# Performance work log

Measured on AMD Instinct MI355X. Metric: run time of the kernel, lower is better.

## Reference

```python
import jax, jax.numpy as jnp
import numpy as np

HIDDEN = 2048
N_HEADS = 32
N_KV_HEADS = 8
N_GROUPS = N_HEADS // N_KV_HEADS  # 4
HEAD_DIM = HIDDEN // N_HEADS      # 64
BATCH, SEQ = 2, 2048


def setup_inputs() -> dict:
    key = jax.random.key(0)
    ks = jax.random.split(key, 5)
    s = 0.02
    return {
        "x": jax.random.normal(ks[0], (BATCH, SEQ, HIDDEN), dtype=jnp.float32),
        "Wq": jax.random.normal(ks[1], (HIDDEN, HIDDEN), dtype=jnp.float32) * s,
        "Wk": jax.random.normal(ks[2], (N_KV_HEADS * HEAD_DIM, HIDDEN), dtype=jnp.float32) * s,
        "Wv": jax.random.normal(ks[3], (N_KV_HEADS * HEAD_DIM, HIDDEN), dtype=jnp.float32) * s,
        "Wo": jax.random.normal(ks[4], (HIDDEN, HIDDEN), dtype=jnp.float32) * s,
    }


def reference(x, Wq, Wk, Wv, Wo):
    b, s, _ = x.shape
    # Projections (nn.Linear: y = x @ W.T)
    q = (x @ Wq.T).reshape(b, s, N_KV_HEADS, N_GROUPS, HEAD_DIM)  # group heads by kv head
    k = (x @ Wk.T).reshape(b, s, N_KV_HEADS, HEAD_DIM)
    v = (x @ Wv.T).reshape(b, s, N_KV_HEADS, HEAD_DIM)
    scale = 1.0 / jnp.sqrt(jnp.asarray(HEAD_DIM, dtype=x.dtype))
    # Grouped scores: equivalent to repeat_interleave of K over groups
    scores = jnp.einsum('bqhgd,bkhd->bhgqk', q, k) * scale  # [b, kvh, g, s, s]
    causal_mask = jnp.triu(jnp.ones((s, s), dtype=bool), k=1)
    scores = jnp.where(causal_mask, -jnp.inf, scores)
    attn = jax.nn.softmax(scores, axis=-1)
    out = jnp.einsum('bhgqk,bkhd->bqhgd', attn, v)  # [b, s, kvh, g, hd]
    out = out.reshape(b, s, HIDDEN)
    return out @ Wo.T
```

## Files before the change

kernel.cpp:

```cpp
#include <hip/hip_runtime.h>

#define HIDDEN 2048
#define NHEADS 32
#define NKV 8
#define HD 64
#define BATCH 2
#define SEQ 2048
#define MROWS (BATCH*SEQ)
#define KVDIM (NKV*HD)
#define QKVN (HIDDEN + 2*KVDIM)

typedef __bf16 bf16x8 __attribute__((ext_vector_type(8)));
typedef float f32x4 __attribute__((ext_vector_type(4)));

__device__ inline void gld16(const __bf16* g, __bf16* l) {
    __builtin_amdgcn_global_load_lds((const __attribute__((address_space(1))) void*)g,
                                     (__attribute__((address_space(3))) void*)l, 16, 0, 0);
}

__global__ __launch_bounds__(256) void cast_all(const float* __restrict__ x,
                                                const float* __restrict__ wq,
                                                const float* __restrict__ wk,
                                                const float* __restrict__ wv,
                                                const float* __restrict__ wo,
                                                __bf16* __restrict__ xb,
                                                __bf16* __restrict__ wqkv,
                                                __bf16* __restrict__ wob,
                                                float qscale) {
    int blk = blockIdx.x;
    const float* src; __bf16* dst; float sc = 1.0f; size_t off;
    if (blk < 8192)        { src = x;  dst = xb;   off = (size_t)blk * 1024; }
    else if (blk < 12288)  { src = wq; dst = wqkv; off = (size_t)(blk - 8192) * 1024; sc = qscale; }
    else if (blk < 13312)  { src = wk; dst = wqkv + (size_t)HIDDEN * HIDDEN; off = (size_t)(blk - 12288) * 1024; }
    else if (blk < 14336)  { src = wv; dst = wqkv + (size_t)(HIDDEN + KVDIM) * HIDDEN; off = (size_t)(blk - 13312) * 1024; }
    else                   { src = wo; dst = wob;  off = (size_t)(blk - 14336) * 1024; }
    size_t i4 = off + (size_t)threadIdx.x * 4;
    float4 f = *(const float4*)(src + i4);
    dst[i4 + 0] = (__bf16)(f.x * sc);
    dst[i4 + 1] = (__bf16)(f.y * sc);
    dst[i4 + 2] = (__bf16)(f.z * sc);
    dst[i4 + 3] = (__bf16)(f.w * sc);
}

__device__ inline void store_val(__bf16* C, size_t idx, float v) { C[idx] = (__bf16)v; }
__device__ inline void store_val(float* C, size_t idx, float v) { C[idx] = v; }

template <typename OutT>
__global__ __launch_bounds__(256) void gemm128(const __bf16* __restrict__ A,
                                               const __bf16* __restrict__ B,
                                               OutT* __restrict__ C,
                                               int M, int N, int K) {
    __shared__ __bf16 As[2][128][32];
    __shared__ __bf16 Bs[2][128][32];
    const int tid  = threadIdx.x;
    const int lane = tid & 63;
    const int w    = tid >> 6;
    const int col  = lane & 15;
    const int quad = lane >> 4;
    const int m0 = blockIdx.y * 128;
    const int n0 = blockIdx.x * 128;
    const int wm = (w >> 1) * 64;
    const int wn = (w & 1) * 64;

    f32x4 acc[4][4];
    #pragma unroll
    for (int i = 0; i < 4; i++)
        #pragma unroll
        for (int j = 0; j < 4; j++) acc[i][j] = (f32x4){0.f,0.f,0.f,0.f};

    const int lrow = lane >> 2;
    const int lcol = (lane & 3) * 8;

    auto stage = [&](int k0, int buf) {
        #pragma unroll
        for (int c = 0; c < 4; c++) {
            int chunk = w * 4 + c;
            if (chunk < 8) {
                const __bf16* g = A + (size_t)(m0 + chunk*16 + lrow) * K + k0 + lcol;
                gld16(g, &As[buf][chunk*16][0]);
            } else {
                int bc = chunk - 8;
                const __bf16* g = B + (size_t)(n0 + bc*16 + lrow) * K + k0 + lcol;
                gld16(g, &Bs[buf][bc*16][0]);
            }
        }
    };

    const int nk = K / 32;
    stage(0, 0);
    for (int ki = 0; ki < nk; ki++) {
        const int buf = ki & 1;
        __syncthreads();
        if (ki + 1 < nk) stage((ki + 1) * 32, buf ^ 1);

        bf16x8 af[4], bfr[4];
        #pragma unroll
        for (int i = 0; i < 4; i++) af[i]  = *(const bf16x8*)&As[buf][wm + i*16 + col][quad*8];
        #pragma unroll
        for (int j = 0; j < 4; j++) bfr[j] = *(const bf16x8*)&Bs[buf][wn + j*16 + col][quad*8];
        #pragma unroll
        for (int i = 0; i < 4; i++)
            #pragma unroll
            for (int j = 0; j < 4; j++)
                acc[i][j] = __builtin_amdgcn_mfma_f32_16x16x32_bf16(af[i], bfr[j], acc[i][j], 0, 0, 0);
    }

    #pragma unroll
    for (int i = 0; i < 4; i++) {
        #pragma unroll
        for (int r = 0; r < 4; r++) {
            int mrow = m0 + wm + i*16 + quad*4 + r;
            size_t base = (size_t)mrow * N + n0 + wn;
            #pragma unroll
            for (int j = 0; j < 4; j++)
                store_val(C, base + j*16 + col, acc[i][j][r]);
        }
    }
}

__global__ __launch_bounds__(256) void transpose_v(const __bf16* __restrict__ QKV,
                                                   __bf16* __restrict__ VT) {
    __shared__ __bf16 tile[64][72];
    const int r0 = blockIdx.x * 64;
    const int s0 = blockIdx.y * 64;
    const int t  = threadIdx.x;
    #pragma unroll
    for (int cc = 0; cc < 2; cc++) {
        int c = t + cc * 256;
        int i = c >> 3;
        int j8 = (c & 7) * 8;
        bf16x8 v = *(const bf16x8*)(QKV + (size_t)(s0 + i) * QKVN + (HIDDEN + KVDIM) + r0 + j8);
        *(bf16x8*)&tile[i][j8] = v;
    }
    __syncthreads();
    #pragma unroll
    for (int cc = 0; cc < 2; cc++) {
        int c = t + cc * 256;
        int d = c >> 3;
        int sc = (c & 7) * 8;
        bf16x8 vv;
        #pragma unroll
        for (int j = 0; j < 8; j++) vv[j] = tile[sc + j][d];
        *(bf16x8*)(VT + (size_t)(r0 + d) * MROWS + s0 + sc) = vv;
    }
}

__global__ __launch_bounds__(256) void flash_attn(const __bf16* __restrict__ QKV,
                                                  const __bf16* __restrict__ VT,
                                                  __bf16* __restrict__ O) {
    const int p    = blockIdx.x & 15;
    const int head = (blockIdx.x >> 4) & 31;
    const int b    = blockIdx.x >> 9;
    const int kvh  = head >> 2;
    const int tid  = threadIdx.x;
    const int lane = tid & 63;
    const int w    = tid >> 6;
    const int col  = lane & 15;
    const int quad = lane >> 4;

    const int qbL = p * 64 + w * 16;
    const int qbH = (31 - p) * 64 + w * 16;
    const int np  = p + 1;
    const int nh  = 32 - p;

    __shared__ __bf16 Ks[2][64][32];
    __shared__ __bf16 Vs[2][64][32];
    __shared__ __bf16 Pt[4][32][72];

    const size_t qL = (size_t)(b * SEQ + qbL + col) * QKVN + head * HD;
    const size_t qH = (size_t)(b * SEQ + qbH + col) * QKVN + head * HD;
    bf16x8 aqL0 = *(const bf16x8*)(QKV + qL + quad * 8);
    bf16x8 aqL1 = *(const bf16x8*)(QKV + qL + 32 + quad * 8);
    bf16x8 aqH0 = *(const bf16x8*)(QKV + qH + quad * 8);
    bf16x8 aqH1 = *(const bf16x8*)(QKV + qH + 32 + quad * 8);

    bf16x8 ones;
    #pragma unroll
    for (int j = 0; j < 8; j++) ones[j] = (__bf16)1.0f;

    f32x4 oL[4], oH[4];
    #pragma unroll
    for (int dn = 0; dn < 4; dn++) { oL[dn] = (f32x4){0.f,0.f,0.f,0.f}; oH[dn] = (f32x4){0.f,0.f,0.f,0.f}; }
    f32x4 lsumL = (f32x4){0.f,0.f,0.f,0.f};
    f32x4 lsumH = (f32x4){0.f,0.f,0.f,0.f};

    const int lrow = lane >> 2;
    const int lcol = (lane & 3) * 8;

    for (int kt = 0; kt < nh; kt++) {
        const int kbase = kt * 64;
        const bool dual = (kt < np);
        __syncthreads();
        #pragma unroll
        for (int c = 0; c < 4; c++) {
            int chunk = w * 4 + c;
            if (chunk < 8) {
                int h = chunk >> 2, rb = chunk & 3;
                const __bf16* g = QKV + (size_t)(b * SEQ + kbase + rb*16 + lrow) * QKVN
                                      + HIDDEN + kvh * HD + h * 32 + lcol;
                gld16(g, &Ks[h][rb*16][0]);
            } else {
                int vc = chunk - 8; int h = vc >> 2, db = vc & 3;
                const __bf16* g = VT + (size_t)(kvh * HD + db*16 + lrow) * MROWS
                                     + b * SEQ + kbase + h * 32 + lcol;
                gld16(g, &Vs[h][db*16][0]);
            }
        }
        __syncthreads();

        f32x4 sH[4], sL[4];
        #pragma unroll
        for (int j = 0; j < 4; j++) { sH[j] = (f32x4){0.f,0.f,0.f,0.f}; sL[j] = (f32x4){0.f,0.f,0.f,0.f}; }
        #pragma unroll
        for (int j = 0; j < 4; j++) {
            bf16x8 bk0 = *(const bf16x8*)&Ks[0][j*16 + col][quad*8];
            bf16x8 bk1 = *(const bf16x8*)&Ks[1][j*16 + col][quad*8];
            sH[j] = __builtin_amdgcn_mfma_f32_16x16x32_bf16(aqH0, bk0, sH[j], 0, 0, 0);
            sH[j] = __builtin_amdgcn_mfma_f32_16x16x32_bf16(aqH1, bk1, sH[j], 0, 0, 0);
            if (dual) {
                sL[j] = __builtin_amdgcn_mfma_f32_16x16x32_bf16(aqL0, bk0, sL[j], 0, 0, 0);
                sL[j] = __builtin_amdgcn_mfma_f32_16x16x32_bf16(aqL1, bk1, sL[j], 0, 0, 0);
            }
        }

        if (kt == nh - 1) {
            #pragma unroll
            for (int r = 0; r < 4; r++) {
                int qrow = qbH + quad*4 + r;
                #pragma unroll
                for (int j = 0; j < 4; j++)
                    if (kbase + j*16 + col > qrow) sH[j][r] = -1e30f;
            }
        }
        if (dual && kt == np - 1) {
            #pragma unroll
            for (int r = 0; r < 4; r++) {
                int qrow = qbL + quad*4 + r;
                #pragma unroll
                for (int j = 0; j < 4; j++)
                    if (kbase + j*16 + col > qrow) sL[j][r] = -1e30f;
            }
        }

        #pragma unroll
        for (int r = 0; r < 4; r++) {
            int pr = quad*4 + r;
            #pragma unroll
            for (int j = 0; j < 4; j++)
                Pt[w][pr][j*16 + col] = (__bf16)__builtin_amdgcn_exp2f(sH[j][r]);
        }
        if (dual) {
            #pragma unroll
            for (int r = 0; r < 4; r++) {
                int pr = quad*4 + r;
                #pragma unroll
                for (int j = 0; j < 4; j++)
                    Pt[w][16 + pr][j*16 + col] = (__bf16)__builtin_amdgcn_exp2f(sL[j][r]);
            }
        }

        __asm__ volatile("s_waitcnt lgkmcnt(0)" ::: "memory");
        bf16x8 apH0 = *(const bf16x8*)&Pt[w][col][quad*8];
        bf16x8 apH1 = *(const bf16x8*)&Pt[w][col][32 + quad*8];
        lsumH = __builtin_amdgcn_mfma_f32_16x16x32_bf16(apH0, ones, lsumH, 0, 0, 0);
        lsumH = __builtin_amdgcn_mfma_f32_16x16x32_bf16(apH1, ones, lsumH, 0, 0, 0);
        bf16x8 apL0, apL1;
        if (dual) {
            apL0 = *(const bf16x8*)&Pt[w][16 + col][quad*8];
            apL1 = *(const bf16x8*)&Pt[w][16 + col][32 + quad*8];
            lsumL = __builtin_amdgcn_mfma_f32_16x16x32_bf16(apL0, ones, lsumL, 0, 0, 0);
            lsumL = __builtin_amdgcn_mfma_f32_16x16x32_bf16(apL1, ones, lsumL, 0, 0, 0);
        }

        #pragma unroll
        for (int dn = 0; dn < 4; dn++) {
            bf16x8 bv0 = *(const bf16x8*)&Vs[0][dn*16 + col][quad*8];
            bf16x8 bv1 = *(const bf16x8*)&Vs[1][dn*16 + col][quad*8];
            oH[dn] = __builtin_amdgcn_mfma_f32_16x16x32_bf16(apH0, bv0, oH[dn], 0, 0, 0);
            oH[dn] = __builtin_amdgcn_mfma_f32_16x16x32_bf16(apH1, bv1, oH[dn], 0, 0, 0);
            if (dual) {
                oL[dn] = __builtin_amdgcn_mfma_f32_16x16x32_bf16(apL0, bv0, oL[dn], 0, 0, 0);
                oL[dn] = __builtin_amdgcn_mfma_f32_16x16x32_bf16(apL1, bv1, oL[dn], 0, 0, 0);
            }
        }
    }

    #pragma unroll
    for (int r = 0; r < 4; r++) {
        float invL = 1.0f / lsumL[r];
        float invH = 1.0f / lsumH[r];
        __bf16* opL = O + (size_t)(b * SEQ + qbL + quad*4 + r) * HIDDEN + head * HD;
        __bf16* opH = O + (size_t)(b * SEQ + qbH + quad*4 + r) * HIDDEN + head * HD;
        #pragma unroll
        for (int dn = 0; dn < 4; dn++) {
            opL[dn*16 + col] = (__bf16)(oL[dn][r] * invL);
            opH[dn*16 + col] = (__bf16)(oH[dn][r] * invH);
        }
    }
}

extern "C" void kernel_launch(void* const* d_in, const int* in_sizes, int n_in,
                              void* d_out, int out_size, void* d_ws, size_t ws_size,
                              hipStream_t stream) {
    const float* x  = (const float*)d_in[0];
    const float* Wq = (const float*)d_in[1];
    const float* Wk = (const float*)d_in[2];
    const float* Wv = (const float*)d_in[3];
    const float* Wo = (const float*)d_in[4];
    float* out = (float*)d_out;

    __bf16* p    = (__bf16*)d_ws;
    __bf16* xb   = p; p += (size_t)MROWS * HIDDEN;
    __bf16* wqkv = p; p += (size_t)QKVN * HIDDEN;
    __bf16* wob  = p; p += (size_t)HIDDEN * HIDDEN;
    __bf16* qkv  = p; p += (size_t)MROWS * QKVN;
    __bf16* vt   = p; p += (size_t)KVDIM * MROWS;
    __bf16* aob  = xb;

    const float qscale = 0.125f * 1.4426950408889634f;
    cast_all<<<18432, 256, 0, stream>>>(x, Wq, Wk, Wv, Wo, xb, wqkv, wob, qscale);

    dim3 blk(256);
    gemm128<__bf16><<<dim3(QKVN/128, MROWS/128), blk, 0, stream>>>(xb, wqkv, qkv, MROWS, QKVN, HIDDEN);
    transpose_v<<<dim3(KVDIM/64, MROWS/64), blk, 0, stream>>>(qkv, vt);
    flash_attn<<<BATCH * NHEADS * (SEQ/128), blk, 0, stream>>>(qkv, vt, aob);
    gemm128<float><<<dim3(HIDDEN/128, MROWS/128), blk, 0, stream>>>(aob, wob, out, MROWS, HIDDEN, HIDDEN);
}
```

Before: 324.9 us.

## Split attention KV loop across two blocks and merge partials in a combine kernel

Each query block's KV tiles are now split between two blocks (even and odd tiles), which doubles the grid for more parallelism and shortens each block's serial loop. Each block writes unnormalized bf16 partial outputs and row sums, and a new combine kernel adds the two partials and normalizes. The score computation is also restructured into a per-phase lambda with a smaller P tile in LDS and an occupancy hint in the launch bounds. The cost is an extra kernel launch, extra global traffic for the partial outputs, and bf16 rounding of the unnormalized partials.

```diff
diff --git a/kernel.cpp b/kernel.cpp
--- a/kernel.cpp
+++ b/kernel.cpp
@@ -145,12 +145,14 @@
     }
 }
 
-__global__ __launch_bounds__(256) void flash_attn(const __bf16* __restrict__ QKV,
-                                                  const __bf16* __restrict__ VT,
-                                                  __bf16* __restrict__ O) {
-    const int p    = blockIdx.x & 15;
-    const int head = (blockIdx.x >> 4) & 31;
-    const int b    = blockIdx.x >> 9;
+__global__ __launch_bounds__(256, 6) void flash_attn(const __bf16* __restrict__ QKV,
+                                                     const __bf16* __restrict__ VT,
+                                                     __bf16* __restrict__ OP,
+                                                     float* __restrict__ LP) {
+    const int e    = blockIdx.x & 1;
+    const int p    = (blockIdx.x >> 1) & 15;
+    const int head = (blockIdx.x >> 5) & 31;
+    const int b    = blockIdx.x >> 10;
     const int kvh  = head >> 2;
     const int tid  = threadIdx.x;
     const int lane = tid & 63;
@@ -165,14 +167,15 @@
 
     __shared__ __bf16 Ks[2][64][32];
     __shared__ __bf16 Vs[2][64][32];
-    __shared__ __bf16 Pt[4][32][72];
-
-    const size_t qL = (size_t)(b * SEQ + qbL + col) * QKVN + head * HD;
-    const size_t qH = (size_t)(b * SEQ + qbH + col) * QKVN + head * HD;
-    bf16x8 aqL0 = *(const bf16x8*)(QKV + qL + quad * 8);
-    bf16x8 aqL1 = *(const bf16x8*)(QKV + qL + 32 + quad * 8);
-    bf16x8 aqH0 = *(const bf16x8*)(QKV + qH + quad * 8);
-    bf16x8 aqH1 = *(const bf16x8*)(QKV + qH + 32 + quad * 8);
+    __shared__ __bf16 Pt[4][16][72];
+
+    const size_t bS = (size_t)b * SEQ;
+    const size_t qLg = (bS + qbL + col) * QKVN + head * HD;
+    const size_t qHg = (bS + qbH + col) * QKVN + head * HD;
+    bf16x8 aqL0 = *(const bf16x8*)(QKV + qLg + quad * 8);
+    bf16x8 aqL1 = *(const bf16x8*)(QKV + qLg + 32 + quad * 8);
+    bf16x8 aqH0 = *(const bf16x8*)(QKV + qHg + quad * 8);
+    bf16x8 aqH1 = *(const bf16x8*)(QKV + qHg + 32 + quad * 8);
 
     bf16x8 ones;
     #pragma unroll
@@ -187,116 +190,116 @@
     const int lrow = lane >> 2;
     const int lcol = (lane & 3) * 8;
 
-    for (int kt = 0; kt < nh; kt++) {
-        const int kbase = kt * 64;
-        const bool dual = (kt < np);
-        __syncthreads();
+    auto stage = [&](int kbase) {
         #pragma unroll
         for (int c = 0; c < 4; c++) {
             int chunk = w * 4 + c;
             if (chunk < 8) {
                 int h = chunk >> 2, rb = chunk & 3;
-                const __bf16* g = QKV + (size_t)(b * SEQ + kbase + rb*16 + lrow) * QKVN
+                const __bf16* g = QKV + (bS + kbase + rb*16 + lrow) * QKVN
                                       + HIDDEN + kvh * HD + h * 32 + lcol;
                 gld16(g, &Ks[h][rb*16][0]);
             } else {
                 int vc = chunk - 8; int h = vc >> 2, db = vc & 3;
                 const __bf16* g = VT + (size_t)(kvh * HD + db*16 + lrow) * MROWS
-                                     + b * SEQ + kbase + h * 32 + lcol;
+                                     + bS + kbase + h * 32 + lcol;
                 gld16(g, &Vs[h][db*16][0]);
             }
         }
-        __syncthreads();
-
-        f32x4 sH[4], sL[4];
-        #pragma unroll
-        for (int j = 0; j < 4; j++) { sH[j] = (f32x4){0.f,0.f,0.f,0.f}; sL[j] = (f32x4){0.f,0.f,0.f,0.f}; }
-        #pragma unroll
-        for (int j = 0; j < 4; j++) {
-            bf16x8 bk0 = *(const bf16x8*)&Ks[0][j*16 + col][quad*8];
-            bf16x8 bk1 = *(const bf16x8*)&Ks[1][j*16 + col][quad*8];
-            sH[j] = __builtin_amdgcn_mfma_f32_16x16x32_bf16(aqH0, bk0, sH[j], 0, 0, 0);
-            sH[j] = __builtin_amdgcn_mfma_f32_16x16x32_bf16(aqH1, bk1, sH[j], 0, 0, 0);
-            if (dual) {
-                sL[j] = __builtin_amdgcn_mfma_f32_16x16x32_bf16(aqL0, bk0, sL[j], 0, 0, 0);
-                sL[j] = __builtin_amdgcn_mfma_f32_16x16x32_bf16(aqL1, bk1, sL[j], 0, 0, 0);
-            }
-        }
-
-        if (kt == nh - 1) {
+    };
+
+    auto phase = [&](bf16x8 aq0, bf16x8 aq1, int qb, bool do_mask, int kbase,
+                     f32x4* o, f32x4& lsum) {
+        #pragma unroll
+        for (int jj = 0; jj < 2; jj++) {
+            f32x4 s[2];
+            s[0] = (f32x4){0.f,0.f,0.f,0.f};
+            s[1] = (f32x4){0.f,0.f,0.f,0.f};
             #pragma unroll
-            for (int r = 0; r < 4; r++) {
-                int qrow = qbH + quad*4 + r;
+            for (int jz = 0; jz < 2; jz++) {
+                int j = jj*2 + jz;
+                bf16x8 bk0 = *(const bf16x8*)&Ks[0][j*16 + col][quad*8];
+                bf16x8 bk1 = *(const bf16x8*)&Ks[1][j*16 + col][quad*8];
+                s[jz] = __builtin_amdgcn_mfma_f32_16x16x32_bf16(aq0, bk0, s[jz], 0, 0, 0);
+                s[jz] = __builtin_amdgcn_mfma_f32_16x16x32_bf16(aq1, bk1, s[jz], 0, 0, 0);
+            }
+            if (do_mask) {
                 #pragma unroll
-                for (int j = 0; j < 4; j++)
-                    if (kbase + j*16 + col > qrow) sH[j][r] = -1e30f;
-            }
-        }
-        if (dual && kt == np - 1) {
-            #pragma unroll
-            for (int r = 0; r < 4; r++) {
-                int qrow = qbL + quad*4 + r;
-                #pragma unroll
-                for (int j = 0; j < 4; j++)
-                    if (kbase + j*16 + col > qrow) sL[j][r] = -1e30f;
-            }
-        }
-
-        #pragma unroll
-        for (int r = 0; r < 4; r++) {
-            int pr = quad*4 + r;
-            #pragma unroll
-            for (int j = 0; j < 4; j++)
-                Pt[w][pr][j*16 + col] = (__bf16)__builtin_amdgcn_exp2f(sH[j][r]);
-        }
-        if (dual) {
+                for (int r = 0; r < 4; r++) {
+                    int qrow = qb + quad*4 + r;
+                    #pragma unroll
+                    for (int jz = 0; jz < 2; jz++)
+                        if (kbase + (jj*2+jz)*16 + col > qrow) s[jz][r] = -1e30f;
+                }
+            }
             #pragma unroll
             for (int r = 0; r < 4; r++) {
                 int pr = quad*4 + r;
-                #pragma unroll
-                for (int j = 0; j < 4; j++)
-                    Pt[w][16 + pr][j*16 + col] = (__bf16)__builtin_amdgcn_exp2f(sL[j][r]);
-            }
-        }
-
+                Pt[w][pr][(jj*2)*16 + col]   = (__bf16)__builtin_amdgcn_exp2f(s[0][r]);
+                Pt[w][pr][(jj*2+1)*16 + col] = (__bf16)__builtin_amdgcn_exp2f(s[1][r]);
+            }
+        }
         __asm__ volatile("s_waitcnt lgkmcnt(0)" ::: "memory");
-        bf16x8 apH0 = *(const bf16x8*)&Pt[w][col][quad*8];
-        bf16x8 apH1 = *(const bf16x8*)&Pt[w][col][32 + quad*8];
-        lsumH = __builtin_amdgcn_mfma_f32_16x16x32_bf16(apH0, ones, lsumH, 0, 0, 0);
-        lsumH = __builtin_amdgcn_mfma_f32_16x16x32_bf16(apH1, ones, lsumH, 0, 0, 0);
-        bf16x8 apL0, apL1;
-        if (dual) {
-            apL0 = *(const bf16x8*)&Pt[w][16 + col][quad*8];
-            apL1 = *(const bf16x8*)&Pt[w][16 + col][32 + quad*8];
-            lsumL = __builtin_amdgcn_mfma_f32_16x16x32_bf16(apL0, ones, lsumL, 0, 0, 0);
-            lsumL = __builtin_amdgcn_mfma_f32_16x16x32_bf16(apL1, ones, lsumL, 0, 0, 0);
-        }
-
+        bf16x8 ap0 = *(const bf16x8*)&Pt[w][col][quad*8];
+        bf16x8 ap1 = *(const bf16x8*)&Pt[w][col][32 + quad*8];
+        lsum = __builtin_amdgcn_mfma_f32_16x16x32_bf16(ap0, ones, lsum, 0, 0, 0);
+        lsum = __builtin_amdgcn_mfma_f32_16x16x32_bf16(ap1, ones, lsum, 0, 0, 0);
         #pragma unroll
         for (int dn = 0; dn < 4; dn++) {
             bf16x8 bv0 = *(const bf16x8*)&Vs[0][dn*16 + col][quad*8];
             bf16x8 bv1 = *(const bf16x8*)&Vs[1][dn*16 + col][quad*8];
-            oH[dn] = __builtin_amdgcn_mfma_f32_16x16x32_bf16(apH0, bv0, oH[dn], 0, 0, 0);
-            oH[dn] = __builtin_amdgcn_mfma_f32_16x16x32_bf16(apH1, bv1, oH[dn], 0, 0, 0);
-            if (dual) {
-                oL[dn] = __builtin_amdgcn_mfma_f32_16x16x32_bf16(apL0, bv0, oL[dn], 0, 0, 0);
-                oL[dn] = __builtin_amdgcn_mfma_f32_16x16x32_bf16(apL1, bv1, oL[dn], 0, 0, 0);
-            }
-        }
-    }
-
+            o[dn] = __builtin_amdgcn_mfma_f32_16x16x32_bf16(ap0, bv0, o[dn], 0, 0, 0);
+            o[dn] = __builtin_amdgcn_mfma_f32_16x16x32_bf16(ap1, bv1, o[dn], 0, 0, 0);
+        }
+    };
+
+    for (int kt = e; kt < nh; kt += 2) {
+        const int kbase = kt * 64;
+        __syncthreads();
+        stage(kbase);
+        __syncthreads();
+        phase(aqH0, aqH1, qbH, kt == nh - 1, kbase, oH, lsumH);
+        if (kt < np)
+            phase(aqL0, aqL1, qbL, kt == np - 1, kbase, oL, lsumL);
+    }
+
+    const size_t eoff = (size_t)e * MROWS * HIDDEN;
     #pragma unroll
     for (int r = 0; r < 4; r++) {
-        float invL = 1.0f / lsumL[r];
-        float invH = 1.0f / lsumH[r];
-        __bf16* opL = O + (size_t)(b * SEQ + qbL + quad*4 + r) * HIDDEN + head * HD;
-        __bf16* opH = O + (size_t)(b * SEQ + qbH + quad*4 + r) * HIDDEN + head * HD;
+        __bf16* opH = OP + eoff + (bS + qbH + quad*4 + r) * HIDDEN + head * HD;
+        __bf16* opL = OP + eoff + (bS + qbL + quad*4 + r) * HIDDEN + head * HD;
         #pragma unroll
         for (int dn = 0; dn < 4; dn++) {
-            opL[dn*16 + col] = (__bf16)(oL[dn][r] * invL);
-            opH[dn*16 + col] = (__bf16)(oH[dn][r] * invH);
-        }
-    }
+            opH[dn*16 + col] = (__bf16)oH[dn][r];
+            opL[dn*16 + col] = (__bf16)oL[dn][r];
+        }
+    }
+    if (col == 0) {
+        float* lp = LP + (size_t)(e * NHEADS + head) * MROWS + bS;
+        #pragma unroll
+        for (int r = 0; r < 4; r++) {
+            lp[qbH + quad*4 + r] = lsumH[r];
+            lp[qbL + quad*4 + r] = lsumL[r];
+        }
+    }
+}
+
+__global__ __launch_bounds__(256) void combine(const __bf16* __restrict__ OP,
+                                               const float* __restrict__ LP,
+                                               __bf16* __restrict__ out) {
+    size_t idx = ((size_t)blockIdx.x * 256 + threadIdx.x) * 8;
+    int g = (int)(idx >> 11);
+    int c = (int)(idx & (HIDDEN - 1));
+    int head = c >> 6;
+    float l = LP[(size_t)head * MROWS + g] + LP[(size_t)(NHEADS + head) * MROWS + g];
+    float inv = 1.0f / l;
+    bf16x8 a = *(const bf16x8*)(OP + idx);
+    bf16x8 bb = *(const bf16x8*)(OP + (size_t)MROWS * HIDDEN + idx);
+    bf16x8 o;
+    #pragma unroll
+    for (int j = 0; j < 8; j++)
+        o[j] = (__bf16)(((float)a[j] + (float)bb[j]) * inv);
+    *(bf16x8*)(out + idx) = o;
 }
 
 extern "C" void kernel_launch(void* const* d_in, const int* in_sizes, int n_in,
@@ -315,6 +318,8 @@
     __bf16* wob  = p; p += (size_t)HIDDEN * HIDDEN;
     __bf16* qkv  = p; p += (size_t)MROWS * QKVN;
     __bf16* vt   = p; p += (size_t)KVDIM * MROWS;
+    __bf16* op   = p; p += (size_t)2 * MROWS * HIDDEN;
+    float*  lp   = (float*)p; p += (size_t)2 * NHEADS * MROWS * 2;
     __bf16* aob  = xb;
 
     const float qscale = 0.125f * 1.4426950408889634f;
@@ -323,6 +328,7 @@
     dim3 blk(256);
     gemm128<__bf16><<<dim3(QKVN/128, MROWS/128), blk, 0, stream>>>(xb, wqkv, qkv, MROWS, QKVN, HIDDEN);
     transpose_v<<<dim3(KVDIM/64, MROWS/64), blk, 0, stream>>>(qkv, vt);
-    flash_attn<<<BATCH * NHEADS * (SEQ/128), blk, 0, stream>>>(qkv, vt, aob);
+    flash_attn<<<2 * BATCH * NHEADS * (SEQ/128), blk, 0, stream>>>(qkv, vt, op, lp);
+    combine<<<(MROWS * HIDDEN) / (256 * 8), blk, 0, stream>>>(op, lp, aob);
     gemm128<float><<<dim3(HIDDEN/128, MROWS/128), blk, 0, stream>>>(aob, wob, out, MROWS, HIDDEN, HIDDEN);
 }
```

After: 373.0 us. 1.15x slower.
